# Optimization experiments

Hardware: AMD Instinct MI355X
Metric: run time of the kernel (lower is better)

Reference implementation:

```python
import jax, jax.numpy as jnp
import numpy as np

B, F, K, DEPTH = 512, 64, 64, 3  # feas == k == 64, deepDepth == 3


def setup_inputs() -> dict:
    key = jax.random.key(0)
    ks = jax.random.split(key, 16)
    x = jax.random.normal(ks[0], (B, F), dtype=jnp.float32)
    # wide: Linear(feas, 1)
    Ww = jax.random.normal(ks[1], (1, F), dtype=jnp.float32) * 0.1
    bw = jnp.zeros((1,), dtype=jnp.float32)
    # cross: Parameter(torch.rand(feas, k))
    cross = jax.random.uniform(ks[2], (F, K), dtype=jnp.float32)
    # attention: Linear(k, k) -> ReLU -> Linear(k, 1, bias=False)
    W1 = jax.random.normal(ks[3], (K, K), dtype=jnp.float32) / np.sqrt(K)
    b1 = jnp.zeros((K,), dtype=jnp.float32)
    w2 = jax.random.normal(ks[4], (K,), dtype=jnp.float32) / np.sqrt(K)
    # deep{i}: Linear(k//i, k//(i+1)) + ReLU, i = 1..DEPTH  -> 64->32->21->16
    dims = [K // i for i in range(1, DEPTH + 2)]  # [64, 32, 21, 16]
    Wd1 = jax.random.normal(ks[5], (dims[1], dims[0]), dtype=jnp.float32) / np.sqrt(dims[0])
    bd1 = jnp.zeros((dims[1],), dtype=jnp.float32)
    Wd2 = jax.random.normal(ks[6], (dims[2], dims[1]), dtype=jnp.float32) / np.sqrt(dims[1])
    bd2 = jnp.zeros((dims[2],), dtype=jnp.float32)
    Wd3 = jax.random.normal(ks[7], (dims[3], dims[2]), dtype=jnp.float32) / np.sqrt(dims[2])
    bd3 = jnp.zeros((dims[3],), dtype=jnp.float32)
    # out: Linear(feas // (deepDepth+1), 1) == Linear(16, 1)
    Wo = jax.random.normal(ks[8], (1, F // (DEPTH + 1)), dtype=jnp.float32) * 0.1
    bo = jnp.zeros((1,), dtype=jnp.float32)
    return {"x": x, "Ww": Ww, "bw": bw, "cross": cross, "W1": W1, "b1": b1,
            "w2": w2, "Wd1": Wd1, "bd1": bd1, "Wd2": Wd2, "bd2": bd2,
            "Wd3": Wd3, "bd3": bd3, "Wo": Wo, "bo": bo}


def reference(x, Ww, bw, cross, W1, b1, w2, Wd1, bd1, Wd2, bd2, Wd3, bd3, Wo, bo):
    linear = x @ Ww.T + bw  # [B, 1]

    # Pairwise FM interactions v[b,i,j,:] = x_i * x_j * (cross_i ∘ cross_j)
    xx = x[:, :, None] * x[:, None, :]                    # [B, F, F]
    cp = cross[:, None, :] * cross[None, :, :]            # [F, F, K]
    v = xx[..., None] * cp[None]                          # [B, F, F, K]

    # attention MLP score per pair
    h = jax.nn.relu(jnp.einsum('bijk,lk->bijl', v, W1) + b1)
    s = jnp.einsum('bijl,l->bij', h, w2)                  # [B, F, F]

    # loop semantics: upper triangle (j >= i), pair kept iff x_i != 0 and x_j != 0
    valid = jnp.triu(jnp.ones((F, F), dtype=bool))[None] \
        & (x[:, :, None] != 0) & (x[:, None, :] != 0)     # [B, F, F]
    neg = jnp.finfo(s.dtype).min
    logits = jnp.where(valid, s, neg)

    # softmax over [0 (seed zeros(1) entry), valid pair scores...];
    # the seed zeros(k) value-vector contributes nothing to the weighted sum.
    m = jnp.maximum(jnp.max(logits, axis=(1, 2)), 0.0)    # [B]
    e = jnp.where(valid, jnp.exp(logits - m[:, None, None]), 0.0)
    denom = jnp.exp(-m) + jnp.sum(e, axis=(1, 2))         # +exp(-m) is the 0-logit term
    tmp = jnp.einsum('bij,bijk->bk', e, v) / denom[:, None]  # [B, K]

    tmp = jax.nn.relu(tmp @ Wd1.T + bd1)
    tmp = jax.nn.relu(tmp @ Wd2.T + bd2)
    tmp = jax.nn.relu(tmp @ Wd3.T + bd3)
    deep_out = tmp @ Wo.T + bo                            # [B, 1]
    return jax.nn.sigmoid(linear + deep_out)
```

## Files before the change

### kernel.cpp

```cpp
#include <hip/hip_runtime.h>
#include <math.h>


#define BB 512
#define FF 64
#define STR 68
#define NPAIRS 2080
#define THREADS 512
#define NIT2 65
#define NEG_BIG -3.402823466e38f

typedef _Float16 half8 __attribute__((ext_vector_type(8)));
typedef _Float16 half4 __attribute__((ext_vector_type(4)));
typedef float f32x4 __attribute__((ext_vector_type(4)));

__device__ __forceinline__ half8 ld8(const _Float16* p) {
    half8 v;
    *(half4*)&v       = *(const half4*)p;
    *((half4*)&v + 1) = *(const half4*)(p + 4);
    return v;
}

__global__ __launch_bounds__(THREADS, 4) void afm_r6_kernel(
    const float* __restrict__ x,
    const float* __restrict__ Ww,
    const float* __restrict__ bw,
    const float* __restrict__ cross,
    const float* __restrict__ W1,
    const float* __restrict__ b1,
    const float* __restrict__ w2,
    const float* __restrict__ Wd1,
    const float* __restrict__ bd1,
    const float* __restrict__ Wd2,
    const float* __restrict__ bd2,
    const float* __restrict__ Wd3,
    const float* __restrict__ bd3,
    const float* __restrict__ Wo,
    const float* __restrict__ bo,
    float* __restrict__ out)
{
    __shared__ __align__(16) _Float16 ah_s [FF * STR];
    __shared__ __align__(16) _Float16 aht_s[FF * STR];
    __shared__ __align__(16) _Float16 M_s  [FF * STR];
    __shared__ float s_s[NPAIRS];
    __shared__ unsigned short lut_s[NPAIRS];
    __shared__ float x_sh[FF];
    __shared__ float part_s[4][FF];
    __shared__ float mlp_s[FF];
    __shared__ float red_s[16];

    const int tid  = threadIdx.x;
    const int lane = tid & 63;
    const int wave = tid >> 6;
    const int b    = blockIdx.x;
    const int m    = lane & 15;
    const int q    = lane >> 4;

    if (tid < FF) x_sh[tid] = x[b * FF + tid];
    __syncthreads();

    for (int idx = tid; idx < FF * FF; idx += THREADS) {
        const int i = idx >> 6, k = idx & 63;
        const _Float16 v = (_Float16)(x_sh[i] * cross[idx]);
        ah_s[i * STR + k]  = v;
        aht_s[k * STR + i] = v;
    }
    for (int idx = tid; idx < (FF * STR) / 2; idx += THREADS)
        ((int*)M_s)[idx] = 0;
    for (int p = tid; p < NPAIRS; p += THREADS) {
        int i = (int)floorf((129.0f - sqrtf(16641.0f - 8.0f * (float)p)) * 0.5f);
        int base = (i * (129 - i)) >> 1;
        if (p < base) { --i; base = (i * (129 - i)) >> 1; }
        else { const int nb = ((i + 1) * (128 - i)) >> 1; if (p >= nb) { ++i; base = nb; } }
        const int j = i + (p - base);
        const int valid = ((x_sh[i] != 0.f) && (x_sh[j] != 0.f)) ? 0x8000 : 0;
        lut_s[p] = (unsigned short)((i << 8) | j | valid);
    }

    half8 afr[4][2];
    #pragma unroll
    for (int mt = 0; mt < 4; ++mt)
        #pragma unroll
        for (int kt = 0; kt < 2; ++kt) {
            const float* wr = W1 + (mt * 16 + m) * FF + kt * 32 + q * 8;
            const f32x4 w0 = *(const f32x4*)wr;
            const f32x4 w1 = *(const f32x4*)(wr + 4);
            half8 h;
            #pragma unroll
            for (int jj = 0; jj < 4; ++jj) {
                h[jj]     = (_Float16)w0[jj];
                h[4 + jj] = (_Float16)w1[jj];
            }
            afr[mt][kt] = h;
        }
    float b1r[16], w2r[16];
    #pragma unroll
    for (int mt = 0; mt < 4; ++mt) {
        const f32x4 bb = *(const f32x4*)(b1 + mt * 16 + q * 4);
        const f32x4 ww = *(const f32x4*)(w2 + mt * 16 + q * 4);
        #pragma unroll
        for (int r = 0; r < 4; ++r) {
            b1r[mt * 4 + r] = bb[r];
            w2r[mt * 4 + r] = ww[r];
        }
    }
    __syncthreads();

    float wave_mx = 0.0f;
    for (int it = wave; it < NIT2; it += 8) {
        const int p0 = it * 32;
        const int ijA = lut_s[p0 + m];
        const int ijB = lut_s[p0 + 16 + m];
        const int iA = (ijA >> 8) & 63, jA = ijA & 63;
        const int iB = (ijB >> 8) & 63, jB = ijB & 63;
        const half8 bA0 = ld8(&ah_s[iA * STR + q * 8])      * ld8(&ah_s[jA * STR + q * 8]);
        const half8 bA1 = ld8(&ah_s[iA * STR + 32 + q * 8]) * ld8(&ah_s[jA * STR + 32 + q * 8]);
        const half8 bB0 = ld8(&ah_s[iB * STR + q * 8])      * ld8(&ah_s[jB * STR + q * 8]);
        const half8 bB1 = ld8(&ah_s[iB * STR + 32 + q * 8]) * ld8(&ah_s[jB * STR + 32 + q * 8]);
        float spA = 0.f, spB = 0.f;
        #pragma unroll
        for (int mt = 0; mt < 4; ++mt) {
            f32x4 aA, aB;
            #pragma unroll
            for (int r = 0; r < 4; ++r) { aA[r] = b1r[mt * 4 + r]; aB[r] = b1r[mt * 4 + r]; }
            aA = __builtin_amdgcn_mfma_f32_16x16x32_f16(afr[mt][0], bA0, aA, 0, 0, 0);
            aB = __builtin_amdgcn_mfma_f32_16x16x32_f16(afr[mt][0], bB0, aB, 0, 0, 0);
            aA = __builtin_amdgcn_mfma_f32_16x16x32_f16(afr[mt][1], bA1, aA, 0, 0, 0);
            aB = __builtin_amdgcn_mfma_f32_16x16x32_f16(afr[mt][1], bB1, aB, 0, 0, 0);
            #pragma unroll
            for (int r = 0; r < 4; ++r) {
                spA = fmaf(w2r[mt * 4 + r], fmaxf(aA[r], 0.f), spA);
                spB = fmaf(w2r[mt * 4 + r], fmaxf(aB[r], 0.f), spB);
            }
        }
        spA += __shfl_xor(spA, 16, 64);
        spA += __shfl_xor(spA, 32, 64);
        spB += __shfl_xor(spB, 16, 64);
        spB += __shfl_xor(spB, 32, 64);
        wave_mx = fmaxf(wave_mx, (ijA & 0x8000) ? spA : 0.f);
        wave_mx = fmaxf(wave_mx, (ijB & 0x8000) ? spB : 0.f);
        if (lane < 16) {
            s_s[p0 + lane]      = spA;
            s_s[p0 + 16 + lane] = spB;
        }
    }
    wave_mx = fmaxf(wave_mx, __shfl_xor(wave_mx, 1, 64));
    wave_mx = fmaxf(wave_mx, __shfl_xor(wave_mx, 2, 64));
    wave_mx = fmaxf(wave_mx, __shfl_xor(wave_mx, 4, 64));
    wave_mx = fmaxf(wave_mx, __shfl_xor(wave_mx, 8, 64));
    if (lane == 0) red_s[wave] = wave_mx;
    __syncthreads();

    float mval = red_s[0];
    #pragma unroll
    for (int w = 1; w < 8; ++w) mval = fmaxf(mval, red_s[w]);

    float sum = 0.f;
    for (int p = tid; p < NPAIRS; p += THREADS) {
        const int ij = lut_s[p];
        const float e = (ij & 0x8000) ? __expf(s_s[p] - mval) : 0.f;
        sum += e;
        M_s[((ij >> 8) & 63) * STR + (ij & 63)] = (_Float16)e;
    }
    #pragma unroll
    for (int off = 32; off > 0; off >>= 1)
        sum += __shfl_xor(sum, off, 64);
    if (lane == 0) red_s[8 + wave] = sum;
    __syncthreads();
    float denom = __expf(-mval);
    #pragma unroll
    for (int w = 0; w < 8; ++w) denom += red_s[8 + w];

    {
        const int t0 = wave * 2;
        #pragma unroll
        for (int t = t0; t < t0 + 2; ++t) {
            const int i0 = (t >> 2) * 16, k0 = (t & 3) * 16;
            const half8 a0  = ld8(&M_s[(i0 + m) * STR + q * 8]);
            const half8 a1  = ld8(&M_s[(i0 + m) * STR + 32 + q * 8]);
            const half8 bb0 = ld8(&aht_s[(k0 + m) * STR + q * 8]);
            const half8 bb1 = ld8(&aht_s[(k0 + m) * STR + 32 + q * 8]);
            f32x4 g = {0.f, 0.f, 0.f, 0.f};
            g = __builtin_amdgcn_mfma_f32_16x16x32_f16(a0, bb0, g, 0, 0, 0);
            g = __builtin_amdgcn_mfma_f32_16x16x32_f16(a1, bb1, g, 0, 0, 0);
            const half4 ap = *(const half4*)&aht_s[(k0 + m) * STR + i0 + q * 4];
            float s4 = (float)ap[0] * g[0] + (float)ap[1] * g[1]
                     + (float)ap[2] * g[2] + (float)ap[3] * g[3];
            s4 += __shfl_xor(s4, 16, 64);
            s4 += __shfl_xor(s4, 32, 64);
            if (lane < 16) part_s[i0 >> 4][k0 + lane] = s4;
        }
    }
    __syncthreads();
    if (tid < FF)
        mlp_s[tid] = (part_s[0][tid] + part_s[1][tid] +
                      part_s[2][tid] + part_s[3][tid]) / denom;
    __syncthreads();

    float* tmp2 = part_s[0];

    {
        const int outi = tid >> 4, kp = tid & 15;
        float a = 0.f;
        #pragma unroll
        for (int t = 0; t < 4; ++t)
            a = fmaf(Wd1[outi * 64 + kp + t * 16], mlp_s[kp + t * 16], a);
        a += __shfl_xor(a, 1, 64);
        a += __shfl_xor(a, 2, 64);
        a += __shfl_xor(a, 4, 64);
        a += __shfl_xor(a, 8, 64);
        if (kp == 0) tmp2[outi] = fmaxf(a + bd1[outi], 0.f);
    }
    __syncthreads();

    if (tid < 21 * 8) {
        const int outi = tid >> 3, kp = tid & 7;
        float a = 0.f;
        #pragma unroll
        for (int t = 0; t < 4; ++t)
            a = fmaf(Wd2[outi * 32 + kp + t * 8], tmp2[kp + t * 8], a);
        a += __shfl_xor(a, 1, 64);
        a += __shfl_xor(a, 2, 64);
        a += __shfl_xor(a, 4, 64);
        if (kp == 0) mlp_s[outi] = fmaxf(a + bd2[outi], 0.f);
    }
    __syncthreads();

    if (tid < 16 * 8) {
        const int outi = tid >> 3, kp = tid & 7;
        float a = Wd3[outi * 21 + kp] * mlp_s[kp];
        a = fmaf(Wd3[outi * 21 + kp + 8], mlp_s[kp + 8], a);
        if (kp < 5) a = fmaf(Wd3[outi * 21 + kp + 16], mlp_s[kp + 16], a);
        a += __shfl_xor(a, 1, 64);
        a += __shfl_xor(a, 2, 64);
        a += __shfl_xor(a, 4, 64);
        if (kp == 0) tmp2[outi] = fmaxf(a + bd3[outi], 0.f);
    }
    __syncthreads();

    if (wave == 0) {
        float v = Ww[lane] * x_sh[lane];
        if (lane < 16) v = fmaf(Wo[lane], tmp2[lane], v);
        #pragma unroll
        for (int off = 32; off > 0; off >>= 1)
            v += __shfl_xor(v, off, 64);
        if (lane == 0) {
            const float z = v + bw[0] + bo[0];
            out[b] = 1.f / (1.f + __expf(-z));
        }
    }
}

extern "C" void kernel_launch(void* const* d_in, const int* in_sizes, int n_in,
                              void* d_out, int out_size, void* d_ws, size_t ws_size,
                              hipStream_t stream) {
    const float* xp    = (const float*)d_in[0];
    const float* Ww    = (const float*)d_in[1];
    const float* bw    = (const float*)d_in[2];
    const float* cross = (const float*)d_in[3];
    const float* W1    = (const float*)d_in[4];
    const float* b1    = (const float*)d_in[5];
    const float* w2    = (const float*)d_in[6];
    const float* Wd1   = (const float*)d_in[7];
    const float* bd1   = (const float*)d_in[8];
    const float* Wd2   = (const float*)d_in[9];
    const float* bd2   = (const float*)d_in[10];
    const float* Wd3   = (const float*)d_in[11];
    const float* bd3   = (const float*)d_in[12];
    const float* Wo    = (const float*)d_in[13];
    const float* bo    = (const float*)d_in[14];
    float* outp = (float*)d_out;

    afm_r6_kernel<<<BB, THREADS, 0, stream>>>(xp, Ww, bw, cross, W1, b1, w2,
                                              Wd1, bd1, Wd2, bd2, Wd3, bd3,
                                              Wo, bo, outp);
}
```

Baseline: 103.3 us.

## Preload tail MLP weights to LDS, prefetch LUT, run tail MLP in one wave

Copies the small deep-MLP weights and biases into shared memory during the prologue, so their global-load latency overlaps the setup phase instead of sitting on the serial tail. The three deep layers and the output are rewritten to run in a single wave using shuffles, which removes several block-wide barriers. The main pair loop prefetches the next LUT entries and splits its accumulations into independent partial sums for more ILP. The cost is extra LDS use (about 12.8 KB), which could limit occupancy, plus a longer prologue.

```diff
diff --git a/kernel.cpp b/kernel.cpp
--- a/kernel.cpp
+++ b/kernel.cpp
@@ -10,6 +10,18 @@
 #define NIT2 65
 #define NEG_BIG -3.402823466e38f
 
+#define WD1_OFF 0
+#define WD2_OFF 2048
+#define WD3_OFF 2720
+#define WO_OFF  3056
+#define BD1_OFF 3072
+#define BD2_OFF 3104
+#define BD3_OFF 3125
+#define WW_OFF  3141
+#define BW_OFF  3205
+#define BO_OFF  3206
+#define WD_TOT  3207
+
 typedef _Float16 half8 __attribute__((ext_vector_type(8)));
 typedef _Float16 half4 __attribute__((ext_vector_type(4)));
 typedef float f32x4 __attribute__((ext_vector_type(4)));
@@ -21,7 +33,7 @@
     return v;
 }
 
-__global__ __launch_bounds__(THREADS, 4) void afm_r6_kernel(
+__global__ __launch_bounds__(THREADS, 4) void afm_r9_kernel(
     const float* __restrict__ x,
     const float* __restrict__ Ww,
     const float* __restrict__ bw,
@@ -46,8 +58,8 @@
     __shared__ unsigned short lut_s[NPAIRS];
     __shared__ float x_sh[FF];
     __shared__ float part_s[4][FF];
-    __shared__ float mlp_s[FF];
     __shared__ float red_s[16];
+    __shared__ __align__(16) float wd_s[WD_TOT + 1];
 
     const int tid  = threadIdx.x;
     const int lane = tid & 63;
@@ -75,6 +87,20 @@
         const int j = i + (p - base);
         const int valid = ((x_sh[i] != 0.f) && (x_sh[j] != 0.f)) ? 0x8000 : 0;
         lut_s[p] = (unsigned short)((i << 8) | j | valid);
+    }
+    for (int idx = tid; idx < WD_TOT; idx += THREADS) {
+        float v;
+        if      (idx < WD2_OFF) v = Wd1[idx];
+        else if (idx < WD3_OFF) v = Wd2[idx - WD2_OFF];
+        else if (idx < WO_OFF)  v = Wd3[idx - WD3_OFF];
+        else if (idx < BD1_OFF) v = Wo[idx - WO_OFF];
+        else if (idx < BD2_OFF) v = bd1[idx - BD1_OFF];
+        else if (idx < BD3_OFF) v = bd2[idx - BD2_OFF];
+        else if (idx < WW_OFF)  v = bd3[idx - BD3_OFF];
+        else if (idx < BW_OFF)  v = Ww[idx - WW_OFF];
+        else if (idx == BW_OFF) v = bw[0];
+        else                    v = bo[0];
+        wd_s[idx] = v;
     }
 
     half8 afr[4][2];
@@ -107,17 +133,28 @@
     __syncthreads();
 
     float wave_mx = 0.0f;
+    int lutA = lut_s[wave * 32 + m];
+    int lutB = lut_s[wave * 32 + 16 + m];
     for (int it = wave; it < NIT2; it += 8) {
         const int p0 = it * 32;
-        const int ijA = lut_s[p0 + m];
-        const int ijB = lut_s[p0 + 16 + m];
-        const int iA = (ijA >> 8) & 63, jA = ijA & 63;
-        const int iB = (ijB >> 8) & 63, jB = ijB & 63;
-        const half8 bA0 = ld8(&ah_s[iA * STR + q * 8])      * ld8(&ah_s[jA * STR + q * 8]);
-        const half8 bA1 = ld8(&ah_s[iA * STR + 32 + q * 8]) * ld8(&ah_s[jA * STR + 32 + q * 8]);
-        const half8 bB0 = ld8(&ah_s[iB * STR + q * 8])      * ld8(&ah_s[jB * STR + q * 8]);
-        const half8 bB1 = ld8(&ah_s[iB * STR + 32 + q * 8]) * ld8(&ah_s[jB * STR + 32 + q * 8]);
-        float spA = 0.f, spB = 0.f;
+        const int iA = (lutA >> 8) & 63, jA = lutA & 63;
+        const int iB = (lutB >> 8) & 63, jB = lutB & 63;
+        const half8 riA0 = ld8(&ah_s[iA * STR + q * 8]);
+        const half8 rjA0 = ld8(&ah_s[jA * STR + q * 8]);
+        const half8 riA1 = ld8(&ah_s[iA * STR + 32 + q * 8]);
+        const half8 rjA1 = ld8(&ah_s[jA * STR + 32 + q * 8]);
+        const half8 riB0 = ld8(&ah_s[iB * STR + q * 8]);
+        const half8 rjB0 = ld8(&ah_s[jB * STR + q * 8]);
+        const half8 riB1 = ld8(&ah_s[iB * STR + 32 + q * 8]);
+        const half8 rjB1 = ld8(&ah_s[jB * STR + 32 + q * 8]);
+        const half8 bA0 = riA0 * rjA0, bA1 = riA1 * rjA1;
+        const half8 bB0 = riB0 * rjB0, bB1 = riB1 * rjB1;
+        const int vA = lutA, vB = lutB;
+        if (it + 8 < NIT2) {
+            lutA = lut_s[(it + 8) * 32 + m];
+            lutB = lut_s[(it + 8) * 32 + 16 + m];
+        }
+        float pA[4], pB[4];
         #pragma unroll
         for (int mt = 0; mt < 4; ++mt) {
             f32x4 aA, aB;
@@ -127,18 +164,22 @@
             aB = __builtin_amdgcn_mfma_f32_16x16x32_f16(afr[mt][0], bB0, aB, 0, 0, 0);
             aA = __builtin_amdgcn_mfma_f32_16x16x32_f16(afr[mt][1], bA1, aA, 0, 0, 0);
             aB = __builtin_amdgcn_mfma_f32_16x16x32_f16(afr[mt][1], bB1, aB, 0, 0, 0);
+            float sA = 0.f, sB = 0.f;
             #pragma unroll
             for (int r = 0; r < 4; ++r) {
-                spA = fmaf(w2r[mt * 4 + r], fmaxf(aA[r], 0.f), spA);
-                spB = fmaf(w2r[mt * 4 + r], fmaxf(aB[r], 0.f), spB);
+                sA = fmaf(w2r[mt * 4 + r], fmaxf(aA[r], 0.f), sA);
+                sB = fmaf(w2r[mt * 4 + r], fmaxf(aB[r], 0.f), sB);
             }
-        }
+            pA[mt] = sA; pB[mt] = sB;
+        }
+        float spA = (pA[0] + pA[1]) + (pA[2] + pA[3]);
+        float spB = (pB[0] + pB[1]) + (pB[2] + pB[3]);
         spA += __shfl_xor(spA, 16, 64);
         spA += __shfl_xor(spA, 32, 64);
         spB += __shfl_xor(spB, 16, 64);
         spB += __shfl_xor(spB, 32, 64);
-        wave_mx = fmaxf(wave_mx, (ijA & 0x8000) ? spA : 0.f);
-        wave_mx = fmaxf(wave_mx, (ijB & 0x8000) ? spB : 0.f);
+        wave_mx = fmaxf(wave_mx, (vA & 0x8000) ? spA : 0.f);
+        wave_mx = fmaxf(wave_mx, (vB & 0x8000) ? spB : 0.f);
         if (lane < 16) {
             s_s[p0 + lane]      = spA;
             s_s[p0 + 16 + lane] = spB;
@@ -192,62 +233,53 @@
         }
     }
     __syncthreads();
-    if (tid < FF)
-        mlp_s[tid] = (part_s[0][tid] + part_s[1][tid] +
-                      part_s[2][tid] + part_s[3][tid]) / denom;
-    __syncthreads();
-
-    float* tmp2 = part_s[0];
-
-    {
-        const int outi = tid >> 4, kp = tid & 15;
-        float a = 0.f;
-        #pragma unroll
-        for (int t = 0; t < 4; ++t)
-            a = fmaf(Wd1[outi * 64 + kp + t * 16], mlp_s[kp + t * 16], a);
-        a += __shfl_xor(a, 1, 64);
-        a += __shfl_xor(a, 2, 64);
-        a += __shfl_xor(a, 4, 64);
-        a += __shfl_xor(a, 8, 64);
-        if (kp == 0) tmp2[outi] = fmaxf(a + bd1[outi], 0.f);
-    }
-    __syncthreads();
-
-    if (tid < 21 * 8) {
-        const int outi = tid >> 3, kp = tid & 7;
-        float a = 0.f;
-        #pragma unroll
-        for (int t = 0; t < 4; ++t)
-            a = fmaf(Wd2[outi * 32 + kp + t * 8], tmp2[kp + t * 8], a);
-        a += __shfl_xor(a, 1, 64);
-        a += __shfl_xor(a, 2, 64);
-        a += __shfl_xor(a, 4, 64);
-        if (kp == 0) mlp_s[outi] = fmaxf(a + bd2[outi], 0.f);
-    }
-    __syncthreads();
-
-    if (tid < 16 * 8) {
-        const int outi = tid >> 3, kp = tid & 7;
-        float a = Wd3[outi * 21 + kp] * mlp_s[kp];
-        a = fmaf(Wd3[outi * 21 + kp + 8], mlp_s[kp + 8], a);
-        if (kp < 5) a = fmaf(Wd3[outi * 21 + kp + 16], mlp_s[kp + 16], a);
-        a += __shfl_xor(a, 1, 64);
-        a += __shfl_xor(a, 2, 64);
-        a += __shfl_xor(a, 4, 64);
-        if (kp == 0) tmp2[outi] = fmaxf(a + bd3[outi], 0.f);
-    }
-    __syncthreads();
-
-    if (wave == 0) {
-        float v = Ww[lane] * x_sh[lane];
-        if (lane < 16) v = fmaf(Wo[lane], tmp2[lane], v);
-        #pragma unroll
-        for (int off = 32; off > 0; off >>= 1)
-            v += __shfl_xor(v, off, 64);
-        if (lane == 0) {
-            const float z = v + bw[0] + bo[0];
-            out[b] = 1.f / (1.f + __expf(-z));
-        }
+
+    if (wave != 0) return;
+
+    const float t64 = (part_s[0][lane] + part_s[1][lane] +
+                       part_s[2][lane] + part_s[3][lane]) / denom;
+
+    const int o1 = lane >> 1, kh = (lane & 1) * 32;
+    float c10 = 0.f, c11 = 0.f, c12 = 0.f, c13 = 0.f;
+    #pragma unroll
+    for (int t = 0; t < 32; t += 4) {
+        c10 = fmaf(wd_s[WD1_OFF + o1 * 64 + kh + t],     __shfl(t64, kh + t, 64),     c10);
+        c11 = fmaf(wd_s[WD1_OFF + o1 * 64 + kh + t + 1], __shfl(t64, kh + t + 1, 64), c11);
+        c12 = fmaf(wd_s[WD1_OFF + o1 * 64 + kh + t + 2], __shfl(t64, kh + t + 2, 64), c12);
+        c13 = fmaf(wd_s[WD1_OFF + o1 * 64 + kh + t + 3], __shfl(t64, kh + t + 3, 64), c13);
+    }
+    float a1 = (c10 + c11) + (c12 + c13);
+    a1 += __shfl_xor(a1, 1, 64);
+    const float h1 = fmaxf(a1 + wd_s[BD1_OFF + o1], 0.f);
+
+    const int o2 = (lane < 21) ? lane : 20;
+    float c20 = 0.f, c21 = 0.f, c22 = 0.f, c23 = 0.f;
+    #pragma unroll
+    for (int t = 0; t < 32; t += 4) {
+        c20 = fmaf(wd_s[WD2_OFF + o2 * 32 + t],     __shfl(h1, 2 * t, 64),       c20);
+        c21 = fmaf(wd_s[WD2_OFF + o2 * 32 + t + 1], __shfl(h1, 2 * (t + 1), 64), c21);
+        c22 = fmaf(wd_s[WD2_OFF + o2 * 32 + t + 2], __shfl(h1, 2 * (t + 2), 64), c22);
+        c23 = fmaf(wd_s[WD2_OFF + o2 * 32 + t + 3], __shfl(h1, 2 * (t + 3), 64), c23);
+    }
+    const float h2 = fmaxf(((c20 + c21) + (c22 + c23)) + wd_s[BD2_OFF + o2], 0.f);
+
+    const int o3 = (lane < 16) ? lane : 15;
+    float c30 = 0.f, c31 = 0.f, c32 = 0.f;
+    #pragma unroll
+    for (int t = 0; t < 21; ++t) {
+        const float pv = fmaf(wd_s[WD3_OFF + o3 * 21 + t], __shfl(h2, t, 64), 0.f);
+        if ((t % 3) == 0) c30 += pv; else if ((t % 3) == 1) c31 += pv; else c32 += pv;
+    }
+    const float h3 = fmaxf((c30 + c31 + c32) + wd_s[BD3_OFF + o3], 0.f);
+
+    float v = wd_s[WW_OFF + lane] * x_sh[lane];
+    if (lane < 16) v = fmaf(wd_s[WO_OFF + lane], h3, v);
+    #pragma unroll
+    for (int off = 32; off > 0; off >>= 1)
+        v += __shfl_xor(v, off, 64);
+    if (lane == 0) {
+        const float z = v + wd_s[BW_OFF] + wd_s[BO_OFF];
+        out[b] = 1.f / (1.f + __expf(-z));
     }
 }
 
@@ -271,7 +303,7 @@
     const float* bo    = (const float*)d_in[14];
     float* outp = (float*)d_out;
 
-    afm_r6_kernel<<<BB, THREADS, 0, stream>>>(xp, Ww, bw, cross, W1, b1, w2,
+    afm_r9_kernel<<<BB, THREADS, 0, stream>>>(xp, Ww, bw, cross, W1, b1, w2,
                                               Wd1, bd1, Wd2, bd2, Wd3, bd3,
                                               Wo, bo, outp);
 }
```

Measured after the change: 106.2 us. 1.03x slower.
